# Performance work log

Measured on AMD Instinct MI355X. Metric: run time of the kernel, lower is better.

## Reference

```python
import jax, jax.numpy as jnp
import numpy as np

B, EVI, L, H, K, NL = 16, 5, 128, 768, 21, 3
SIGMA = 0.1

def _kernel_mus(n):
    mu = [1.0]
    bin_size = 2.0 / (n - 1)
    mu.append(1 - bin_size / 2)
    for i in range(1, n - 1):
        mu.append(mu[i] - bin_size)
    return mu

MU = np.asarray(_kernel_mus(K), dtype=np.float32)                      # [K]
SIG = np.asarray([0.001] + [SIGMA] * (K - 1), dtype=np.float32)        # [K]


def setup_inputs() -> dict:
    key = jax.random.key(0)
    ks = jax.random.split(key, 8)
    std = 0.02
    inputs_hiddens = jax.random.normal(ks[0], (B, EVI, L, H), jnp.float32)
    inputs = jax.random.normal(ks[1], (B, EVI, H), jnp.float32)
    # mask_text: valid tokens with CLS (position 0) zeroed, as in torch forward
    mask_text = jnp.ones((B, EVI, L), jnp.float32).at[:, :, 0].set(0.0)
    seg = (jnp.arange(L) >= L // 2).astype(jnp.float32)  # first half = claim, second = evidence
    mask_claim = (1.0 - seg) * mask_text
    mask_evidence = seg * mask_text
    return {
        "inputs_hiddens": inputs_hiddens,
        "inputs": inputs,
        "mask_text": mask_text,
        "mask_claim": mask_claim,
        "mask_evidence": mask_evidence,
        "W_att": jax.random.normal(ks[2], (K, 1), jnp.float32) * std,
        "b_att": jnp.zeros((1,), jnp.float32),
        "W_sel": jax.random.normal(ks[3], (K, 1), jnp.float32) * std,
        "b_sel": jnp.zeros((1,), jnp.float32),
        "gat_W1": jax.random.normal(ks[4], (2 * H, 128), jnp.float32) * std,
        "gat_b1": jnp.zeros((128,), jnp.float32),
        "gat_W2": jax.random.normal(ks[5], (128, 1), jnp.float32) * std,
        "gat_b2": jnp.zeros((1,), jnp.float32),
        "inf_W": jax.random.normal(ks[6], (2 * H, NL), jnp.float32) * std,
        "inf_b": jnp.zeros((NL,), jnp.float32),
    }


def _l2norm(x):
    # F.normalize(p=2, dim=-1) with eps=1e-12
    return x / jnp.maximum(jnp.linalg.norm(x, axis=-1, keepdims=True), 1e-12)


def _kernel_pool(sim, attn_d):
    # sim: [N, Lq, Ld]; attn_d: [N, Ld]  ->  [N, Lq, K]
    # exp(-(sim - mu)^2 / (2 sigma^2)) masked by doc attention, summed over doc tokens
    pv = jnp.exp(-((sim[..., None] - MU) ** 2) / (2.0 * SIG ** 2)) * attn_d[:, None, :, None]
    return pv.sum(axis=2)


def _intersect_att(qn, dn, attn_q, attn_d, W_att, b_att):
    # token-level attention scores over q tokens: [N, Lq]
    sim = jnp.einsum('nqh,ndh->nqd', qn, dn)
    lp = jnp.log(jnp.maximum(_kernel_pool(sim, attn_d), 1e-10))  # [N, Lq, K]
    lp = (lp @ W_att + b_att)[..., 0]                            # [N, Lq]
    lp = jnp.where(attn_q == 0.0, -1e4, lp)
    return jax.nn.softmax(lp, axis=1)


def _intersect_sel(qn, dn, attn_q, attn_d, W_sel, b_sel):
    # per-pair evidence selection logit: [N, 1]
    sim = jnp.einsum('nqh,ndh->nqd', qn, dn)
    lp = jnp.log(jnp.maximum(_kernel_pool(sim, attn_d), 1e-10)) * attn_q[..., None] * 0.01
    lp = lp.sum(axis=1) / (attn_q.sum(axis=1, keepdims=True) + 1e-10)  # [N, K]
    return lp @ W_sel + b_sel


def _gat(x, W1, b1, W2, b2):
    # proj_gat: Linear(2H,128) -> ReLU -> Linear(128,1)
    return jnp.maximum(x @ W1 + b1, 0.0) @ W2 + b2


def reference(inputs_hiddens, inputs, mask_text, mask_claim, mask_evidence,
              W_att, b_att, W_sel, b_sel, gat_W1, gat_b1, gat_W2, gat_b2,
              inf_W, inf_b):
    hid = inputs_hiddens                          # [B, EVI, L, H]
    hn = _l2norm(hid)
    hn_flat = hn.reshape(-1, L, H)

    # evidence selection prior over EVI pieces
    sel = _intersect_sel(hn_flat, hn_flat,
                         mask_claim.reshape(-1, L), mask_evidence.reshape(-1, L),
                         W_sel, b_sel)
    select_prob = jax.nn.softmax(sel.reshape(B, EVI, 1), axis=1)

    att_de = []
    for i in range(EVI):  # fixed small structural loop
        own_n = hn[:, i]                           # [B, L, H]
        own_mask = mask_text[:, i]                 # [B, L]
        dn = jnp.broadcast_to(own_n[:, None], (B, EVI, L, H)).reshape(-1, L, H)
        dm = jnp.broadcast_to(own_mask[:, None], (B, EVI, L)).reshape(-1, L)
        att = _intersect_att(hn_flat, dn, mask_evidence.reshape(-1, L), dm, W_att, b_att)
        att = att.reshape(B, EVI, L, 1)
        denoise = (att * hid).sum(axis=2)          # [B, EVI, H]
        own_inp = jnp.broadcast_to(inputs[:, i:i + 1], (B, EVI, H))
        w_de = jax.nn.softmax(_gat(jnp.concatenate([own_inp, denoise], -1),
                                   gat_W1, gat_b1, gat_W2, gat_b2), axis=1)  # [B, EVI, 1]
        att_de.append((denoise * w_de).sum(axis=1))  # [B, H]

    att_de = jnp.stack(att_de, axis=1)             # [B, EVI, H]
    feats = jnp.concatenate([inputs, att_de], axis=-1)  # [B, EVI, 2H]
    class_prob = jax.nn.softmax(feats @ inf_W + inf_b, axis=2)
    prob = jnp.log((select_prob * class_prob).sum(axis=1))  # [B, NL]
    return prob
```

## Files before the change

kernel.cpp:

```cpp
#include <hip/hip_runtime.h>
#include <math.h>

#define NB 16
#define NE 5
#define LL 128
#define HH 768
#define NK 21
#define NCLS 3
#define NN (NB*NE)

typedef float f32x4 __attribute__((ext_vector_type(4)));
typedef float f32x8 __attribute__((ext_vector_type(8)));
typedef short s16x8 __attribute__((ext_vector_type(8)));

__device__ __forceinline__ short bf16rne(float f) {
    union { float f; unsigned u; } c; c.f = f;
    unsigned u = c.u;
    unsigned r = (u + 0x7FFFu + ((u >> 16) & 1u)) >> 16;
    return (short)r;
}
__device__ __forceinline__ float sum8(f32x8 x) {
    return ((x[0] + x[1]) + (x[2] + x[3])) + ((x[4] + x[5]) + (x[6] + x[7]));
}
__device__ __forceinline__ f32x8 exp2v(f32x8 x) {
// ... 22 lines not shown
        const int bb = blockIdx.x - 640;
        const int tI = bb >> 1, jI = bb & 1;
        #pragma unroll
        for (int i = 0; i < 16; ++i) {
            const int r = (tid >> 6) + i * 4, c = tid & 63;
            sT[r][c] = W1[(size_t)(tI * 64 + r) * 128 + jI * 64 + c];
        }
        __syncthreads();
        #pragma unroll
        for (int i = 0; i < 16; ++i) {
            const int r = (tid >> 6) + i * 4, c = tid & 63;
            w1t[(size_t)(jI * 64 + r) * 1536 + tI * 64 + c] = sT[c][r];
        }
        return;
    }
    const int n = blockIdx.x >> 3, slab = blockIdx.x & 7;
    const int l = tid & 63, w = tid >> 6;
    float* sInv = &sT[0][0];
    #pragma unroll
    for (int rr = 0; rr < 4; ++rr) {
        const int lr = w * 4 + rr;
        const int row = slab * 16 + lr;
        const float4* rp = reinterpret_cast<const float4*>(hid + ((size_t)n * LL + row) * HH);
        float4 a = rp[l], b = rp[l + 64], c = rp[l + 128];
        float ss = a.x*a.x + a.y*a.y + a.z*a.z + a.w*a.w
                 + b.x*b.x + b.y*b.y + b.z*b.z + b.w*b.w
                 + c.x*c.x + c.y*c.y + c.z*c.z + c.w*c.w;
        #pragma unroll
        for (int o = 32; o > 0; o >>= 1) ss += __shfl_xor(ss, o, 64);
        if (l == 0) sInv[lr] = 1.0f / fmaxf(sqrtf(ss), 1e-12f);
    }
    __syncthreads();
    const float* base = hid + (size_t)n * LL * HH;
    s16x8* dst = reinterpret_cast<s16x8*>(hswz) + (size_t)n * 12288;
    #pragma unroll
    for (int i = 0; i < 6; ++i) {
        const int uid = i * 256 + tid;
        const int s = uid >> 6, sub = uid & 63;
        const int r15 = sub >> 2, kc = sub & 3;
        const int row = slab * 16 + r15;
        const int k0 = s * 32 + kc * 8;
        const float4* p = reinterpret_cast<const float4*>(base + (size_t)row * HH + k0);
        float4 v0 = p[0], v1 = p[1];
        const float inv = sInv[r15];
        s16x8 h;
        h[0] = bf16rne(v0.x * inv); h[1] = bf16rne(v0.y * inv);
        h[2] = bf16rne(v0.z * inv); h[3] = bf16rne(v0.w * inv);
        h[4] = bf16rne(v1.x * inv); h[5] = bf16rne(v1.y * inv);
        h[6] = bf16rne(v1.z * inv); h[7] = bf16rne(v1.w * inv);
        dst[(size_t)s * 512 + slab * 64 + kc * 16 + r15] = h;
    }
}

__global__ __launch_bounds__(256, 2) void k_simpool(
    const short* __restrict__ hswz,
    const float* __restrict__ mask_text, const float* __restrict__ mask_claim,
    const float* __restrict__ mask_evidence,
    const float* __restrict__ W_att, const float* __restrict__ b_att,
    const float* __restrict__ W_sel,
    float* __restrict__ attw, float2* __restrict__ dselPart)
{
    const int bid = blockIdx.x;
    const int b = bid & 15, rest = bid >> 4;
    const int pair = rest >> 1, qh = rest & 1;
    const int e = pair / NE, ep = pair - e * NE;
    const int nq = b * NE + e, nd = b * NE + ep;
    const bool diag = (e == ep);
    const int tid = threadIdx.x, lane = tid & 63, w = tid >> 6;
    const int lx = lane & 15, lg = lane >> 4;
    const int rw = w & 1, cw = w >> 1;

    __shared__ s16x8 sB[2][1024];
    __shared__ __align__(16) float sMT[LL];
    __shared__ __align__(16) float sMEd[LL];
    __shared__ float sMEq[64], sMCq[64], sSel[64];
    __shared__ float sWA[NK], sWS[NK], sCK[NK];

    if (tid < 128) {
        sMT[tid]  = mask_text[nd * LL + tid];
        sMEd[tid] = mask_evidence[nd * LL + tid];
    } else if (tid < 192) {
        const int q = tid - 128;
        sMEq[q] = mask_evidence[nq * LL + qh * 64 + q];
        sMCq[q] = mask_claim[nq * LL + qh * 64 + q];
    } else if (tid < 192 + NK) {
        sWA[tid - 192] = W_att[tid - 192] * 0.69314718f;
    } else if (tid < 213 + NK) {
        sWS[tid - 213] = W_sel[tid - 213] * 0.69314718f;
    } else if (tid < 254) {
        const int k = tid - 233;
        const float kk = (float)(k - 1);
        sCK[k] = exp2f(fmaf(kk, 13.7056029f, fmaf(kk * kk, -0.72134752f, -32.0f)));
    } else if (tid == 254) {
        sCK[0] = 1.0f;
    }

    const s16x8* gA = reinterpret_cast<const s16x8*>(hswz) + (size_t)nq * 12288;
    const s16x8* gB = reinterpret_cast<const s16x8*>(hswz) + (size_t)nd * 12288;

    const int rt0 = (qh * 4 + rw * 2) * 64;
    const int rt1 = rt0 + 64;

    {
        s16x8 t0 = gB[tid], t1 = gB[tid + 256], t2 = gB[tid + 512], t3 = gB[tid + 768];
        sB[0][tid] = t0; sB[0][tid + 256] = t1;
        sB[0][tid + 512] = t2; sB[0][tid + 768] = t3;
    }
    s16x8 a00 = gA[rt0 + lane],       a01 = gA[512 + rt0 + lane];
    s16x8 a10 = gA[rt1 + lane],       a11 = gA[512 + rt1 + lane];

    f32x4 acc[2][4];
    #pragma unroll
    for (int mi = 0; mi < 2; ++mi)
        #pragma unroll
        for (int j = 0; j < 4; ++j) acc[mi][j] = (f32x4){0.f, 0.f, 0.f, 0.f};

    __syncthreads();

    const int cb = cw * 256;
    for (int s = 0; s < 12; ++s) {
        const int cur = s & 1;
        s16x8 nB0, nB1, nB2, nB3, n00, n01, n10, n11;
        if (s < 11) {
            const s16x8* gBs = gB + (s + 1) * 1024;
            nB0 = gBs[tid]; nB1 = gBs[tid + 256];
            nB2 = gBs[tid + 512]; nB3 = gBs[tid + 768];
            const s16x8* gAs = gA + (s + 1) * 1024;
            n00 = gAs[rt0 + lane]; n01 = gAs[512 + rt0 + lane];
            n10 = gAs[rt1 + lane]; n11 = gAs[512 + rt1 + lane];
        }
        #pragma unroll
        for (int j = 0; j < 4; ++j) {
            s16x8 b0 = sB[cur][cb + j * 64 + lane];
            acc[0][j] = __builtin_amdgcn_mfma_f32_16x16x32_bf16(a00, b0, acc[0][j], 0, 0, 0);
            acc[1][j] = __builtin_amdgcn_mfma_f32_16x16x32_bf16(a10, b0, acc[1][j], 0, 0, 0);
        }
        #pragma unroll
        for (int j = 0; j < 4; ++j) {
            s16x8 b1 = sB[cur][512 + cb + j * 64 + lane];
            acc[0][j] = __builtin_amdgcn_mfma_f32_16x16x32_bf16(a01, b1, acc[0][j], 0, 0, 0);
            acc[1][j] = __builtin_amdgcn_mfma_f32_16x16x32_bf16(a11, b1, acc[1][j], 0, 0, 0);
        }
        if (s < 11) {
            sB[1 - cur][tid] = nB0; sB[1 - cur][tid + 256] = nB1;
            sB[1 - cur][tid + 512] = nB2; sB[1 - cur][tid + 768] = nB3;
            a00 = n00; a01 = n01; a10 = n10; a11 = n11;
            __syncthreads();
        }
    }

    __syncthreads();
    float* sS = reinterpret_cast<float*>(sB);
    {
        #pragma unroll
        for (int mi = 0; mi < 2; ++mi) {
            #pragma unroll
            for (int j = 0; j < 4; ++j) {
                const int col = cw * 64 + j * 16 + lx;
                const int uu = col >> 2, ce = col & 3;
                #pragma unroll
                for (int r = 0; r < 4; ++r) {
                    const int row = rw * 32 + mi * 16 + lg * 4 + r;
                    sS[row * 128 + ((uu ^ (row & 31)) << 2) + ce] = acc[mi][j][r];
                }
            }
        }
    }
    __syncthreads();

    const int row = w * 16 + (lane & 15);
    const int sl  = lane >> 4;
    const int rx  = row & 31;
    const float4* rp = reinterpret_cast<const float4*>(sS + row * 128);

    float pk[NK], vk[NK];
    #pragma unroll
    for (int k = 0; k < NK; ++k) { pk[k] = 0.f; vk[k] = 0.f; }

    #pragma unroll
    for (int c = 0; c < 4; ++c) {
        const float4 va = rp[(sl * 8 + c * 2) ^ rx];
        const float4 vb = rp[(sl * 8 + c * 2 + 1) ^ rx];
        const f32x8 s = mk8(va, vb);
        const int j0 = sl * 32 + c * 8;
        const f32x8 m = mk8(*reinterpret_cast<const float4*>(&sMT[j0]),
                            *reinterpret_cast<const float4*>(&sMT[j0 + 4]));
        f32x8 d = s - 1.0f;
        const f32x8 g = exp2v(d * d * -721347.52f);
        pk[0] += sum8(m * g);
        const f32x8 t = exp2v(s * -14.4269504f);
        d = s - 0.95f;
        const f32x8 P = exp2v(d * d * -72.134752f + 32.0f);
        f32x8 u = m * P;
        pk[1] += sum8(u);
        #pragma unroll
        for (int k = 2; k <= 20; ++k) { u *= t; pk[k] += sum8(u); }
        if (diag) {
            const f32x8 me = mk8(*reinterpret_cast<const float4*>(&sMEd[j0]),
                                 *reinterpret_cast<const float4*>(&sMEd[j0 + 4]));
            f32x8 uv = me * P;
            vk[0] += sum8(me * g);
            vk[1] += sum8(uv);
            #pragma unroll
            for (int k = 2; k <= 20; ++k) { uv *= t; vk[k] += sum8(uv); }
        }
    }
    #pragma unroll
    for (int k = 0; k < NK; ++k) {
        pk[k] += __shfl_xor(pk[k], 16, 64);
        pk[k] += __shfl_xor(pk[k], 32, 64);
    }
    if (diag) {
        #pragma unroll
        for (int k = 0; k < NK; ++k) {
            vk[k] += __shfl_xor(vk[k], 16, 64);
            vk[k] += __shfl_xor(vk[k], 32, 64);
        }
    }
    const float bAtt = b_att[0];
    float lgt = bAtt;
    #pragma unroll
    for (int k = 0; k < NK; ++k)
        lgt = fmaf(sWA[k], log2f(fmaxf(pk[k] * sCK[k], 1e-10f)), lgt);
    if (sl == 0) {
        const size_t obase = ((size_t)ep * NN + nq) * LL + qh * 64;
        attw[obase + row] = (sMEq[row] == 0.0f) ? -10000.0f : lgt;
    }
    if (diag) {
        float rv = 0.f;
        #pragma unroll
        for (int k = 0; k < NK; ++k)
            rv = fmaf(sWS[k], log2f(fmaxf(vk[k] * sCK[k], 1e-10f)), rv);
        if (sl == 0) sSel[row] = sMCq[row] * rv;
        __syncthreads();
        if (tid < 64) {
            float su = sSel[tid], ms = sMCq[tid];
            #pragma unroll
            for (int o = 32; o > 0; o >>= 1) {
                su += __shfl_xor(su, o, 64);
                ms += __shfl_xor(ms, o, 64);
            }
            if (tid == 0) dselPart[nq * 2 + qh] = make_float2(su, ms);
        }
    }
}

__global__ __launch_bounds__(256) void k_denoise(
    const float* __restrict__ hid, const float* __restrict__ attw,
    float* __restrict__ denoi)
{
    const int blk = blockIdx.x;
    const int nq = blk / 3, ch = blk - nq * 3;
    const int tid = threadIdx.x, l = tid & 63, g = tid >> 6;
    __shared__ float sA[NE][LL];
    __shared__ f32x4 sP[4][NE][64];
    for (int ep = g; ep < NE; ep += 4) {
        const float* ap = attw + ((size_t)ep * NN + nq) * LL;
        float a0 = ap[l], a1 = ap[l + 64];
        float m = fmaxf(a0, a1);
        #pragma unroll
        for (int o = 32; o > 0; o >>= 1) m = fmaxf(m, __shfl_xor(m, o, 64));
        float e0 = __expf(a0 - m), e1 = __expf(a1 - m);
        float s = e0 + e1;
        #pragma unroll
        for (int o = 32; o > 0; o >>= 1) s += __shfl_xor(s, o, 64);
        float inv = 1.0f / s;
        sA[ep][l] = e0 * inv;
        sA[ep][l + 64] = e1 * inv;
    }
    __syncthreads();
    const int h = ch * 256 + l * 4;
    const f32x4* hp = reinterpret_cast<const f32x4*>(hid + (size_t)nq * LL * HH + h);
    f32x4 p0 = {0,0,0,0}, p1 = {0,0,0,0}, p2 = {0,0,0,0}, p3 = {0,0,0,0}, p4 = {0,0,0,0};
    #pragma unroll 8
    for (int q = 0; q < 32; ++q) {
        const int qq = g * 32 + q;
        const f32x4 x = hp[(size_t)qq * (HH / 4)];
        p0 += sA[0][qq] * x;
        p1 += sA[1][qq] * x;
        p2 += sA[2][qq] * x;
        p3 += sA[3][qq] * x;
        p4 += sA[4][qq] * x;
    }
    sP[g][0][l] = p0; sP[g][1][l] = p1; sP[g][2][l] = p2;
    sP[g][3][l] = p3; sP[g][4][l] = p4;
    __syncthreads();
    if (tid < 64) {
        #define DNST(EP) { \
            f32x4 r = sP[0][EP][l] + sP[1][EP][l] + sP[2][EP][l] + sP[3][EP][l]; \
            *reinterpret_cast<f32x4*>(denoi + ((size_t)(EP) * NN + nq) * HH + h) = r; }
        DNST(0) DNST(1) DNST(2) DNST(3) DNST(4)
        #undef DNST
    }
}

// ... 126 lines not shown
    float d0, d1, d2, d3, d4;
#define DSEL(I, D) { float2 pa = dselPart[(b * NE + (I)) * 2], pb = dselPart[(b * NE + (I)) * 2 + 1]; \
                     (D) = bs + 0.01f * (pa.x + pb.x) / ((pa.y + pb.y) + 1e-10f); }
    DSEL(0, d0) DSEL(1, d1) DSEL(2, d2) DSEL(3, d3) DSEL(4, d4)
#undef DSEL
    float m = fmaxf(fmaxf(fmaxf(d0, d1), fmaxf(d2, d3)), d4);
    float s0 = __expf(d0 - m), s1 = __expf(d1 - m), s2 = __expf(d2 - m);
    float s3 = __expf(d3 - m), s4 = __expf(d4 - m);
    float sinv = 1.0f / (s0 + s1 + s2 + s3 + s4);
    float sp0 = s0 * sinv, sp1 = s1 * sinv, sp2 = s2 * sinv, sp3 = s3 * sinv, sp4 = s4 * sinv;
    float acc0 = 0.f, acc1 = 0.f, acc2 = 0.f;
#define CMB(I, SP) { \
        float l0 = logi[(b * NE + (I)) * NCLS], l1 = logi[(b * NE + (I)) * NCLS + 1], \
              l2 = logi[(b * NE + (I)) * NCLS + 2]; \
        float mm = fmaxf(fmaxf(l0, l1), l2); \
        float e0 = __expf(l0 - mm), e1 = __expf(l1 - mm), e2 = __expf(l2 - mm); \
        float si = 1.0f / (e0 + e1 + e2); \
        acc0 += (SP) * e0 * si; acc1 += (SP) * e1 * si; acc2 += (SP) * e2 * si; }
    CMB(0, sp0) CMB(1, sp1) CMB(2, sp2) CMB(3, sp3) CMB(4, sp4)
#undef CMB
    out[b * NCLS + 0] = logf(acc0);
    out[b * NCLS + 1] = logf(acc1);
    out[b * NCLS + 2] = logf(acc2);
}

extern "C" void kernel_launch(void* const* d_in, const int* in_sizes, int n_in,
                              void* d_out, int out_size, void* d_ws, size_t ws_size,
                              hipStream_t stream) {
    (void)in_sizes; (void)n_in; (void)out_size; (void)ws_size;
    const float* hid           = (const float*)d_in[0];
    const float* inputs        = (const float*)d_in[1];
    const float* mask_text     = (const float*)d_in[2];
    const float* mask_claim    = (const float*)d_in[3];
    const float* mask_evidence = (const float*)d_in[4];
    const float* W_att  = (const float*)d_in[5];
    const float* b_att  = (const float*)d_in[6];
    const float* W_sel  = (const float*)d_in[7];
    const float* b_sel  = (const float*)d_in[8];
    const float* gat_W1 = (const float*)d_in[9];
    const float* gat_b1 = (const float*)d_in[10];
    const float* gat_W2 = (const float*)d_in[11];
    const float* gat_b2 = (const float*)d_in[12];
    const float* inf_W  = (const float*)d_in[13];
    const float* inf_b  = (const float*)d_in[14];
    (void)gat_b2;

    short* hswz  = (short*)d_ws;
    float* denoi = (float*)((char*)d_ws + 15728640);
    float* attw  = denoi + 307200;
    float2* dselPart = (float2*)(attw + 51200);
    float* w1t   = (float*)(dselPart + 160);
    float* part  = w1t + 196608;
    float* logi  = part + 25600;

    k_prep<<<688, 256, 0, stream>>>(hid, hswz, gat_W1, w1t);
    k_simpool<<<800, 256, 0, stream>>>(hswz, mask_text, mask_claim, mask_evidence,
                                       W_att, b_att, W_sel, attw, dselPart);
    k_denoise<<<NN * 3, 256, 0, stream>>>(hid, attw, denoi);
    k_gat2<<<800, 256, 0, stream>>>(inputs, denoi, w1t, gat_b1, gat_W2, part);
    k_logits<<<NN, 256, 0, stream>>>(inputs, denoi, part, inf_W, inf_b, logi);
    k_combine<<<1, 64, 0, stream>>>(dselPart, b_sel, logi, (float*)d_out);
}
```

Baseline: 81.67 us.

## Split fused similarity GEMM and kernel pooling into two separate kernels

Splits the fused k_simpool kernel in two. k_gemm computes the bf16 MFMA similarity tiles and writes them to a global scratch buffer, and k_pool reads them back to do the Gaussian kernel pooling and logits. The intent is to stop the GEMM's register and LDS pressure from capping occupancy in the exp-heavy pooling phase, and to let each kernel get its own launch bounds. The cost is an extra launch plus a round trip of about 6.5 MB of fp32 similarities through global memory or L2.

```diff
diff --git a/kernel.cpp b/kernel.cpp
--- a/kernel.cpp
+++ b/kernel.cpp
@@ -98,8 +98,105 @@
     }
 }
 
-__global__ __launch_bounds__(256, 2) void k_simpool(
-    const short* __restrict__ hswz,
+__global__ __launch_bounds__(256, 2) void k_gemm(
+    const short* __restrict__ hswz, float* __restrict__ sims)
+{
+    const int bid = blockIdx.x;
+    const int b = bid & 15, rest = bid >> 4;
+    const int pair = rest >> 1, qh = rest & 1;
+    const int e = pair / NE, ep = pair - e * NE;
+    const int nq = b * NE + e, nd = b * NE + ep;
+    const int tid = threadIdx.x, lane = tid & 63, w = tid >> 6;
+    const int lx = lane & 15, lg = lane >> 4;
+    const int rw = w & 1, cw = w >> 1;
+
+    __shared__ s16x8 sB[2][1024];
+
+    const s16x8* gA = reinterpret_cast<const s16x8*>(hswz) + (size_t)nq * 12288;
+    const s16x8* gB = reinterpret_cast<const s16x8*>(hswz) + (size_t)nd * 12288;
+
+    const int rt0 = (qh * 4 + rw * 2) * 64;
+    const int rt1 = rt0 + 64;
+
+    {
+        s16x8 t0 = gB[tid], t1 = gB[tid + 256], t2 = gB[tid + 512], t3 = gB[tid + 768];
+        sB[0][tid] = t0; sB[0][tid + 256] = t1;
+        sB[0][tid + 512] = t2; sB[0][tid + 768] = t3;
+    }
+    s16x8 a00 = gA[rt0 + lane],       a01 = gA[512 + rt0 + lane];
+    s16x8 a10 = gA[rt1 + lane],       a11 = gA[512 + rt1 + lane];
+
+    f32x4 acc[2][4];
+    #pragma unroll
+    for (int mi = 0; mi < 2; ++mi)
+        #pragma unroll
+        for (int j = 0; j < 4; ++j) acc[mi][j] = (f32x4){0.f, 0.f, 0.f, 0.f};
+
+    __syncthreads();
+
+    const int cb = cw * 256;
+    for (int s = 0; s < 12; ++s) {
+        const int cur = s & 1;
+        s16x8 nB0, nB1, nB2, nB3, n00, n01, n10, n11;
+        if (s < 11) {
+            const s16x8* gBs = gB + (s + 1) * 1024;
+            nB0 = gBs[tid]; nB1 = gBs[tid + 256];
+            nB2 = gBs[tid + 512]; nB3 = gBs[tid + 768];
+            const s16x8* gAs = gA + (s + 1) * 1024;
+            n00 = gAs[rt0 + lane]; n01 = gAs[512 + rt0 + lane];
+            n10 = gAs[rt1 + lane]; n11 = gAs[512 + rt1 + lane];
+        }
+        #pragma unroll
+        for (int j = 0; j < 4; ++j) {
+            s16x8 b0 = sB[cur][cb + j * 64 + lane];
+            acc[0][j] = __builtin_amdgcn_mfma_f32_16x16x32_bf16(a00, b0, acc[0][j], 0, 0, 0);
+            acc[1][j] = __builtin_amdgcn_mfma_f32_16x16x32_bf16(a10, b0, acc[1][j], 0, 0, 0);
+        }
+        #pragma unroll
+        for (int j = 0; j < 4; ++j) {
+            s16x8 b1 = sB[cur][512 + cb + j * 64 + lane];
+            acc[0][j] = __builtin_amdgcn_mfma_f32_16x16x32_bf16(a01, b1, acc[0][j], 0, 0, 0);
+            acc[1][j] = __builtin_amdgcn_mfma_f32_16x16x32_bf16(a11, b1, acc[1][j], 0, 0, 0);
+        }
+        if (s < 11) {
+            sB[1 - cur][tid] = nB0; sB[1 - cur][tid + 256] = nB1;
+            sB[1 - cur][tid + 512] = nB2; sB[1 - cur][tid + 768] = nB3;
+            a00 = n00; a01 = n01; a10 = n10; a11 = n11;
+            __syncthreads();
+        }
+    }
+
+    __syncthreads();
+    float* sS = reinterpret_cast<float*>(sB);
+    {
+        #pragma unroll
+        for (int mi = 0; mi < 2; ++mi) {
+            #pragma unroll
+            for (int j = 0; j < 4; ++j) {
+                const int col = cw * 64 + j * 16 + lx;
+                const int uu = col >> 2, ce = col & 3;
+                #pragma unroll
+                for (int r = 0; r < 4; ++r) {
+                    const int row = rw * 32 + mi * 16 + lg * 4 + r;
+                    sS[row * 128 + ((uu ^ (row & 31)) << 2) + ce] = acc[mi][j][r];
+                }
+            }
+        }
+    }
+    __syncthreads();
+    float4* gs = reinterpret_cast<float4*>(sims) + (size_t)bid * 2048;
+    #pragma unroll
+    for (int k = 0; k < 8; ++k) {
+        const int q = tid + k * 256;
+        const int row = q >> 5, uu = q & 31;
+        const float4 v = *reinterpret_cast<const float4*>(
+            &sS[row * 128 + ((uu ^ (row & 31)) << 2)]);
+        gs[q] = v;
+    }
+}
+
+__global__ __launch_bounds__(256) void k_pool(
+    const float* __restrict__ sims,
     const float* __restrict__ mask_text, const float* __restrict__ mask_claim,
     const float* __restrict__ mask_evidence,
     const float* __restrict__ W_att, const float* __restrict__ b_att,
@@ -113,10 +210,7 @@
     const int nq = b * NE + e, nd = b * NE + ep;
     const bool diag = (e == ep);
     const int tid = threadIdx.x, lane = tid & 63, w = tid >> 6;
-    const int lx = lane & 15, lg = lane >> 4;
-    const int rw = w & 1, cw = w >> 1;
-
-    __shared__ s16x8 sB[2][1024];
+
     __shared__ __align__(16) float sMT[LL];
     __shared__ __align__(16) float sMEd[LL];
     __shared__ float sMEq[64], sMCq[64], sSel[64];
@@ -140,84 +234,12 @@
     } else if (tid == 254) {
         sCK[0] = 1.0f;
     }
-
-    const s16x8* gA = reinterpret_cast<const s16x8*>(hswz) + (size_t)nq * 12288;
-    const s16x8* gB = reinterpret_cast<const s16x8*>(hswz) + (size_t)nd * 12288;
-
-    const int rt0 = (qh * 4 + rw * 2) * 64;
-    const int rt1 = rt0 + 64;
-
-    {
-        s16x8 t0 = gB[tid], t1 = gB[tid + 256], t2 = gB[tid + 512], t3 = gB[tid + 768];
-        sB[0][tid] = t0; sB[0][tid + 256] = t1;
-        sB[0][tid + 512] = t2; sB[0][tid + 768] = t3;
-    }
-    s16x8 a00 = gA[rt0 + lane],       a01 = gA[512 + rt0 + lane];
-    s16x8 a10 = gA[rt1 + lane],       a11 = gA[512 + rt1 + lane];
-
-    f32x4 acc[2][4];
-    #pragma unroll
-    for (int mi = 0; mi < 2; ++mi)
-        #pragma unroll
-        for (int j = 0; j < 4; ++j) acc[mi][j] = (f32x4){0.f, 0.f, 0.f, 0.f};
-
-    __syncthreads();
-
-    const int cb = cw * 256;
-    for (int s = 0; s < 12; ++s) {
-        const int cur = s & 1;
-        s16x8 nB0, nB1, nB2, nB3, n00, n01, n10, n11;
-        if (s < 11) {
-            const s16x8* gBs = gB + (s + 1) * 1024;
-            nB0 = gBs[tid]; nB1 = gBs[tid + 256];
-            nB2 = gBs[tid + 512]; nB3 = gBs[tid + 768];
-            const s16x8* gAs = gA + (s + 1) * 1024;
-            n00 = gAs[rt0 + lane]; n01 = gAs[512 + rt0 + lane];
-            n10 = gAs[rt1 + lane]; n11 = gAs[512 + rt1 + lane];
-        }
-        #pragma unroll
-        for (int j = 0; j < 4; ++j) {
-            s16x8 b0 = sB[cur][cb + j * 64 + lane];
-            acc[0][j] = __builtin_amdgcn_mfma_f32_16x16x32_bf16(a00, b0, acc[0][j], 0, 0, 0);
-            acc[1][j] = __builtin_amdgcn_mfma_f32_16x16x32_bf16(a10, b0, acc[1][j], 0, 0, 0);
-        }
-        #pragma unroll
-        for (int j = 0; j < 4; ++j) {
-            s16x8 b1 = sB[cur][512 + cb + j * 64 + lane];
-            acc[0][j] = __builtin_amdgcn_mfma_f32_16x16x32_bf16(a01, b1, acc[0][j], 0, 0, 0);
-            acc[1][j] = __builtin_amdgcn_mfma_f32_16x16x32_bf16(a11, b1, acc[1][j], 0, 0, 0);
-        }
-        if (s < 11) {
-            sB[1 - cur][tid] = nB0; sB[1 - cur][tid + 256] = nB1;
-            sB[1 - cur][tid + 512] = nB2; sB[1 - cur][tid + 768] = nB3;
-            a00 = n00; a01 = n01; a10 = n10; a11 = n11;
-            __syncthreads();
-        }
-    }
-
-    __syncthreads();
-    float* sS = reinterpret_cast<float*>(sB);
-    {
-        #pragma unroll
-        for (int mi = 0; mi < 2; ++mi) {
-            #pragma unroll
-            for (int j = 0; j < 4; ++j) {
-                const int col = cw * 64 + j * 16 + lx;
-                const int uu = col >> 2, ce = col & 3;
-                #pragma unroll
-                for (int r = 0; r < 4; ++r) {
-                    const int row = rw * 32 + mi * 16 + lg * 4 + r;
-                    sS[row * 128 + ((uu ^ (row & 31)) << 2) + ce] = acc[mi][j][r];
-                }
-            }
-        }
-    }
-    __syncthreads();
-
-    const int row = w * 16 + (lane & 15);
-    const int sl  = lane >> 4;
-    const int rx  = row & 31;
-    const float4* rp = reinterpret_cast<const float4*>(sS + row * 128);
+    __syncthreads();
+
+    const int row = w * 16 + (lane >> 2);
+    const int sl  = lane & 3;
+    const float4* rp4 = reinterpret_cast<const float4*>(sims)
+                      + (size_t)bid * 2048 + row * 32;
 
     float pk[NK], vk[NK];
     #pragma unroll
@@ -225,8 +247,8 @@
 
     #pragma unroll
     for (int c = 0; c < 4; ++c) {
-        const float4 va = rp[(sl * 8 + c * 2) ^ rx];
-        const float4 vb = rp[(sl * 8 + c * 2 + 1) ^ rx];
+        const float4 va = rp4[sl * 8 + c * 2];
+        const float4 vb = rp4[sl * 8 + c * 2 + 1];
         const f32x8 s = mk8(va, vb);
         const int j0 = sl * 32 + c * 8;
         const f32x8 m = mk8(*reinterpret_cast<const float4*>(&sMT[j0]),
@@ -253,14 +275,14 @@
     }
     #pragma unroll
     for (int k = 0; k < NK; ++k) {
-        pk[k] += __shfl_xor(pk[k], 16, 64);
-        pk[k] += __shfl_xor(pk[k], 32, 64);
+        pk[k] += __shfl_xor(pk[k], 1, 64);
+        pk[k] += __shfl_xor(pk[k], 2, 64);
     }
     if (diag) {
         #pragma unroll
         for (int k = 0; k < NK; ++k) {
-            vk[k] += __shfl_xor(vk[k], 16, 64);
-            vk[k] += __shfl_xor(vk[k], 32, 64);
+            vk[k] += __shfl_xor(vk[k], 1, 64);
+            vk[k] += __shfl_xor(vk[k], 2, 64);
         }
     }
     const float bAtt = b_att[0];
@@ -519,10 +541,12 @@
     float* w1t   = (float*)(dselPart + 160);
     float* part  = w1t + 196608;
     float* logi  = part + 25600;
+    float* sims  = logi + 256;
 
     k_prep<<<688, 256, 0, stream>>>(hid, hswz, gat_W1, w1t);
-    k_simpool<<<800, 256, 0, stream>>>(hswz, mask_text, mask_claim, mask_evidence,
-                                       W_att, b_att, W_sel, attw, dselPart);
+    k_gemm<<<800, 256, 0, stream>>>(hswz, sims);
+    k_pool<<<800, 256, 0, stream>>>(sims, mask_text, mask_claim, mask_evidence,
+                                    W_att, b_att, W_sel, attw, dselPart);
     k_denoise<<<NN * 3, 256, 0, stream>>>(hid, attw, denoi);
     k_gat2<<<800, 256, 0, stream>>>(inputs, denoi, w1t, gat_b1, gat_W2, part);
     k_logits<<<NN, 256, 0, stream>>>(inputs, denoi, part, inf_W, inf_b, logi);
```

Result: slower. 90.36 us (+10.6%).

## Process both query halves per block in simpool to reuse staged doc tiles

Applied to the files above, without the earlier changes.

Each k_simpool block now computes all 128 query rows for a (batch, query-evidence, doc-evidence) triple instead of one 64-row half. The grid halves from 800 to 400 blocks. Each block keeps twice as many MFMA accumulators and A fragments, then runs the kernel-pooling epilogue in two phases through the same shared buffer. This halves the global loads and LDS staging of the document B tiles. The cost is higher register pressure under launch_bounds(256,2), fewer blocks to spread over the CUs, and a longer serial epilogue per block.

```diff
diff --git a/kernel.cpp b/kernel.cpp
--- a/kernel.cpp
+++ b/kernel.cpp
@@ -107,8 +107,7 @@
     float* __restrict__ attw, float2* __restrict__ dselPart)
 {
     const int bid = blockIdx.x;
-    const int b = bid & 15, rest = bid >> 4;
-    const int pair = rest >> 1, qh = rest & 1;
+    const int b = bid & 15, pair = bid >> 4;
     const int e = pair / NE, ep = pair - e * NE;
     const int nq = b * NE + e, nd = b * NE + ep;
     const bool diag = (e == ep);
@@ -119,174 +118,192 @@
     __shared__ s16x8 sB[2][1024];
     __shared__ __align__(16) float sMT[LL];
     __shared__ __align__(16) float sMEd[LL];
-    __shared__ float sMEq[64], sMCq[64], sSel[64];
+    __shared__ float sMEq[LL], sMCq[LL], sSel[64];
     __shared__ float sWA[NK], sWS[NK], sCK[NK];
 
     if (tid < 128) {
         sMT[tid]  = mask_text[nd * LL + tid];
         sMEd[tid] = mask_evidence[nd * LL + tid];
-    } else if (tid < 192) {
+    } else {
         const int q = tid - 128;
-        sMEq[q] = mask_evidence[nq * LL + qh * 64 + q];
-        sMCq[q] = mask_claim[nq * LL + qh * 64 + q];
-    } else if (tid < 192 + NK) {
-        sWA[tid - 192] = W_att[tid - 192] * 0.69314718f;
-    } else if (tid < 213 + NK) {
-        sWS[tid - 213] = W_sel[tid - 213] * 0.69314718f;
-    } else if (tid < 254) {
-        const int k = tid - 233;
+        sMEq[q] = mask_evidence[nq * LL + q];
+        sMCq[q] = mask_claim[nq * LL + q];
+    }
+    if (tid < NK) {
+        sWA[tid] = W_att[tid] * 0.69314718f;
+    } else if (tid < 2 * NK) {
+        sWS[tid - NK] = W_sel[tid - NK] * 0.69314718f;
+    } else if (tid < 62) {
+        const int k = tid - 41;
         const float kk = (float)(k - 1);
         sCK[k] = exp2f(fmaf(kk, 13.7056029f, fmaf(kk * kk, -0.72134752f, -32.0f)));
-    } else if (tid == 254) {
+    } else if (tid == 62) {
         sCK[0] = 1.0f;
     }
 
     const s16x8* gA = reinterpret_cast<const s16x8*>(hswz) + (size_t)nq * 12288;
     const s16x8* gB = reinterpret_cast<const s16x8*>(hswz) + (size_t)nd * 12288;
 
-    const int rt0 = (qh * 4 + rw * 2) * 64;
-    const int rt1 = rt0 + 64;
+    const int rt00 = (rw * 2) * 64,     rt01 = rt00 + 64;
+    const int rt10 = (4 + rw * 2) * 64, rt11 = rt10 + 64;
 
     {
         s16x8 t0 = gB[tid], t1 = gB[tid + 256], t2 = gB[tid + 512], t3 = gB[tid + 768];
         sB[0][tid] = t0; sB[0][tid + 256] = t1;
         sB[0][tid + 512] = t2; sB[0][tid + 768] = t3;
     }
-    s16x8 a00 = gA[rt0 + lane],       a01 = gA[512 + rt0 + lane];
-    s16x8 a10 = gA[rt1 + lane],       a11 = gA[512 + rt1 + lane];
-
-    f32x4 acc[2][4];
-    #pragma unroll
-    for (int mi = 0; mi < 2; ++mi)
-        #pragma unroll
-        for (int j = 0; j < 4; ++j) acc[mi][j] = (f32x4){0.f, 0.f, 0.f, 0.f};
+    s16x8 a000 = gA[rt00 + lane], a001 = gA[512 + rt00 + lane];
+    s16x8 a010 = gA[rt01 + lane], a011 = gA[512 + rt01 + lane];
+    s16x8 a100 = gA[rt10 + lane], a101 = gA[512 + rt10 + lane];
+    s16x8 a110 = gA[rt11 + lane], a111 = gA[512 + rt11 + lane];
+
+    f32x4 acc[2][2][4];
+    #pragma unroll
+    for (int h = 0; h < 2; ++h)
+        #pragma unroll
+        for (int mi = 0; mi < 2; ++mi)
+            #pragma unroll
+            for (int j = 0; j < 4; ++j) acc[h][mi][j] = (f32x4){0.f, 0.f, 0.f, 0.f};
 
     __syncthreads();
 
     const int cb = cw * 256;
     for (int s = 0; s < 12; ++s) {
         const int cur = s & 1;
-        s16x8 nB0, nB1, nB2, nB3, n00, n01, n10, n11;
+        s16x8 nB0, nB1, nB2, nB3;
+        s16x8 n000, n001, n010, n011, n100, n101, n110, n111;
         if (s < 11) {
             const s16x8* gBs = gB + (s + 1) * 1024;
             nB0 = gBs[tid]; nB1 = gBs[tid + 256];
             nB2 = gBs[tid + 512]; nB3 = gBs[tid + 768];
             const s16x8* gAs = gA + (s + 1) * 1024;
-            n00 = gAs[rt0 + lane]; n01 = gAs[512 + rt0 + lane];
-            n10 = gAs[rt1 + lane]; n11 = gAs[512 + rt1 + lane];
+            n000 = gAs[rt00 + lane]; n001 = gAs[512 + rt00 + lane];
+            n010 = gAs[rt01 + lane]; n011 = gAs[512 + rt01 + lane];
+            n100 = gAs[rt10 + lane]; n101 = gAs[512 + rt10 + lane];
+            n110 = gAs[rt11 + lane]; n111 = gAs[512 + rt11 + lane];
         }
         #pragma unroll
         for (int j = 0; j < 4; ++j) {
-            s16x8 b0 = sB[cur][cb + j * 64 + lane];
-            acc[0][j] = __builtin_amdgcn_mfma_f32_16x16x32_bf16(a00, b0, acc[0][j], 0, 0, 0);
-            acc[1][j] = __builtin_amdgcn_mfma_f32_16x16x32_bf16(a10, b0, acc[1][j], 0, 0, 0);
+            s16x8 bf = sB[cur][cb + j * 64 + lane];
+            acc[0][0][j] = __builtin_amdgcn_mfma_f32_16x16x32_bf16(a000, bf, acc[0][0][j], 0, 0, 0);
+            acc[0][1][j] = __builtin_amdgcn_mfma_f32_16x16x32_bf16(a010, bf, acc[0][1][j], 0, 0, 0);
+            acc[1][0][j] = __builtin_amdgcn_mfma_f32_16x16x32_bf16(a100, bf, acc[1][0][j], 0, 0, 0);
+            acc[1][1][j] = __builtin_amdgcn_mfma_f32_16x16x32_bf16(a110, bf, acc[1][1][j], 0, 0, 0);
         }
         #pragma unroll
         for (int j = 0; j < 4; ++j) {
-            s16x8 b1 = sB[cur][512 + cb + j * 64 + lane];
-            acc[0][j] = __builtin_amdgcn_mfma_f32_16x16x32_bf16(a01, b1, acc[0][j], 0, 0, 0);
-            acc[1][j] = __builtin_amdgcn_mfma_f32_16x16x32_bf16(a11, b1, acc[1][j], 0, 0, 0);
+            s16x8 bf = sB[cur][512 + cb + j * 64 + lane];
+            acc[0][0][j] = __builtin_amdgcn_mfma_f32_16x16x32_bf16(a001, bf, acc[0][0][j], 0, 0, 0);
+            acc[0][1][j] = __builtin_amdgcn_mfma_f32_16x16x32_bf16(a011, bf, acc[0][1][j], 0, 0, 0);
+            acc[1][0][j] = __builtin_amdgcn_mfma_f32_16x16x32_bf16(a101, bf, acc[1][0][j], 0, 0, 0);
+            acc[1][1][j] = __builtin_amdgcn_mfma_f32_16x16x32_bf16(a111, bf, acc[1][1][j], 0, 0, 0);
         }
         if (s < 11) {
             sB[1 - cur][tid] = nB0; sB[1 - cur][tid + 256] = nB1;
             sB[1 - cur][tid + 512] = nB2; sB[1 - cur][tid + 768] = nB3;
-            a00 = n00; a01 = n01; a10 = n10; a11 = n11;
+            a000 = n000; a001 = n001; a010 = n010; a011 = n011;
+            a100 = n100; a101 = n101; a110 = n110; a111 = n111;
             __syncthreads();
         }
     }
 
-    __syncthreads();
     float* sS = reinterpret_cast<float*>(sB);
-    {
-        #pragma unroll
-        for (int mi = 0; mi < 2; ++mi) {
+    const float bAtt = b_att[0];
+    const size_t obase = ((size_t)ep * NN + nq) * LL;
+
+    #pragma unroll
+    for (int ph = 0; ph < 2; ++ph) {
+        __syncthreads();
+        {
             #pragma unroll
-            for (int j = 0; j < 4; ++j) {
-                const int col = cw * 64 + j * 16 + lx;
-                const int uu = col >> 2, ce = col & 3;
+            for (int mi = 0; mi < 2; ++mi) {
                 #pragma unroll
-                for (int r = 0; r < 4; ++r) {
-                    const int row = rw * 32 + mi * 16 + lg * 4 + r;
-                    sS[row * 128 + ((uu ^ (row & 31)) << 2) + ce] = acc[mi][j][r];
+                for (int j = 0; j < 4; ++j) {
+                    const int col = cw * 64 + j * 16 + lx;
+                    const int uu = col >> 2, ce = col & 3;
+                    #pragma unroll
+                    for (int r = 0; r < 4; ++r) {
+                        const int row = rw * 32 + mi * 16 + lg * 4 + r;
+                        const f32x4 av = (ph == 0) ? acc[0][mi][j] : acc[1][mi][j];
+                        sS[row * 128 + ((uu ^ (row & 31)) << 2) + ce] = av[r];
+                    }
                 }
             }
         }
-    }
-    __syncthreads();
-
-    const int row = w * 16 + (lane & 15);
-    const int sl  = lane >> 4;
-    const int rx  = row & 31;
-    const float4* rp = reinterpret_cast<const float4*>(sS + row * 128);
-
-    float pk[NK], vk[NK];
-    #pragma unroll
-    for (int k = 0; k < NK; ++k) { pk[k] = 0.f; vk[k] = 0.f; }
-
-    #pragma unroll
-    for (int c = 0; c < 4; ++c) {
-        const float4 va = rp[(sl * 8 + c * 2) ^ rx];
-        const float4 vb = rp[(sl * 8 + c * 2 + 1) ^ rx];
-        const f32x8 s = mk8(va, vb);
-        const int j0 = sl * 32 + c * 8;
-        const f32x8 m = mk8(*reinterpret_cast<const float4*>(&sMT[j0]),
-                            *reinterpret_cast<const float4*>(&sMT[j0 + 4]));
-        f32x8 d = s - 1.0f;
-        const f32x8 g = exp2v(d * d * -721347.52f);
-        pk[0] += sum8(m * g);
-        const f32x8 t = exp2v(s * -14.4269504f);
-        d = s - 0.95f;
-        const f32x8 P = exp2v(d * d * -72.134752f + 32.0f);
-        f32x8 u = m * P;
-        pk[1] += sum8(u);
-        #pragma unroll
-        for (int k = 2; k <= 20; ++k) { u *= t; pk[k] += sum8(u); }
+        __syncthreads();
+
+        const int row = w * 16 + (lane & 15);
+        const int sl  = lane >> 4;
+        const int rx  = row & 31;
+        const int grow = ph * 64 + row;
+        const float4* rp = reinterpret_cast<const float4*>(sS + row * 128);
+
+        float pk[NK], vk[NK];
+        #pragma unroll
+        for (int k = 0; k < NK; ++k) { pk[k] = 0.f; vk[k] = 0.f; }
+
+        #pragma unroll
+        for (int c = 0; c < 4; ++c) {
+            const float4 va = rp[(sl * 8 + c * 2) ^ rx];
+            const float4 vb = rp[(sl * 8 + c * 2 + 1) ^ rx];
+            const f32x8 s = mk8(va, vb);
+            const int j0 = sl * 32 + c * 8;
+            const f32x8 m = mk8(*reinterpret_cast<const float4*>(&sMT[j0]),
+                                *reinterpret_cast<const float4*>(&sMT[j0 + 4]));
+            f32x8 d = s - 1.0f;
+            const f32x8 g = exp2v(d * d * -721347.52f);
+            pk[0] += sum8(m * g);
+            const f32x8 t = exp2v(s * -14.4269504f);
+            d = s - 0.95f;
+            const f32x8 P = exp2v(d * d * -72.134752f + 32.0f);
+            f32x8 u = m * P;
+            pk[1] += sum8(u);
+            #pragma unroll
+            for (int k = 2; k <= 20; ++k) { u *= t; pk[k] += sum8(u); }
+            if (diag) {
+                const f32x8 me = mk8(*reinterpret_cast<const float4*>(&sMEd[j0]),
+                                     *reinterpret_cast<const float4*>(&sMEd[j0 + 4]));
+                f32x8 uv = me * P;
+                vk[0] += sum8(me * g);
+                vk[1] += sum8(uv);
+                #pragma unroll
+                for (int k = 2; k <= 20; ++k) { uv *= t; vk[k] += sum8(uv); }
+            }
+        }
+        #pragma unroll
+        for (int k = 0; k < NK; ++k) {
+            pk[k] += __shfl_xor(pk[k], 16, 64);
+            pk[k] += __shfl_xor(pk[k], 32, 64);
+        }
         if (diag) {
-            const f32x8 me = mk8(*reinterpret_cast<const float4*>(&sMEd[j0]),
-                                 *reinterpret_cast<const float4*>(&sMEd[j0 + 4]));
-            f32x8 uv = me * P;
-            vk[0] += sum8(me * g);
-            vk[1] += sum8(uv);
             #pragma unroll
-            for (int k = 2; k <= 20; ++k) { uv *= t; vk[k] += sum8(uv); }
-        }
-    }
-    #pragma unroll
-    for (int k = 0; k < NK; ++k) {
-        pk[k] += __shfl_xor(pk[k], 16, 64);
-        pk[k] += __shfl_xor(pk[k], 32, 64);
-    }
-    if (diag) {
-        #pragma unroll
-        for (int k = 0; k < NK; ++k) {
-            vk[k] += __shfl_xor(vk[k], 16, 64);
-            vk[k] += __shfl_xor(vk[k], 32, 64);
-        }
-    }
-    const float bAtt = b_att[0];
-    float lgt = bAtt;
-    #pragma unroll
-    for (int k = 0; k < NK; ++k)
-        lgt = fmaf(sWA[k], log2f(fmaxf(pk[k] * sCK[k], 1e-10f)), lgt);
-    if (sl == 0) {
-        const size_t obase = ((size_t)ep * NN + nq) * LL + qh * 64;
-        attw[obase + row] = (sMEq[row] == 0.0f) ? -10000.0f : lgt;
-    }
-    if (diag) {
-        float rv = 0.f;
+            for (int k = 0; k < NK; ++k) {
+                vk[k] += __shfl_xor(vk[k], 16, 64);
+                vk[k] += __shfl_xor(vk[k], 32, 64);
+            }
+        }
+        float lgt = bAtt;
         #pragma unroll
         for (int k = 0; k < NK; ++k)
-            rv = fmaf(sWS[k], log2f(fmaxf(vk[k] * sCK[k], 1e-10f)), rv);
-        if (sl == 0) sSel[row] = sMCq[row] * rv;
-        __syncthreads();
-        if (tid < 64) {
-            float su = sSel[tid], ms = sMCq[tid];
+            lgt = fmaf(sWA[k], log2f(fmaxf(pk[k] * sCK[k], 1e-10f)), lgt);
+        if (sl == 0)
+            attw[obase + grow] = (sMEq[grow] == 0.0f) ? -10000.0f : lgt;
+        if (diag) {
+            float rv = 0.f;
             #pragma unroll
-            for (int o = 32; o > 0; o >>= 1) {
-                su += __shfl_xor(su, o, 64);
-                ms += __shfl_xor(ms, o, 64);
+            for (int k = 0; k < NK; ++k)
+                rv = fmaf(sWS[k], log2f(fmaxf(vk[k] * sCK[k], 1e-10f)), rv);
+            if (sl == 0) sSel[row] = sMCq[grow] * rv;
+            __syncthreads();
+            if (tid < 64) {
+                float su = sSel[tid], ms = sMCq[ph * 64 + tid];
+                #pragma unroll
+                for (int o = 32; o > 0; o >>= 1) {
+                    su += __shfl_xor(su, o, 64);
+                    ms += __shfl_xor(ms, o, 64);
+                }
+                if (tid == 0) dselPart[nq * 2 + ph] = make_float2(su, ms);
             }
-            if (tid == 0) dselPart[nq * 2 + qh] = make_float2(su, ms);
         }
     }
 }
@@ -521,7 +538,7 @@
     float* logi  = part + 25600;
 
     k_prep<<<688, 256, 0, stream>>>(hid, hswz, gat_W1, w1t);
-    k_simpool<<<800, 256, 0, stream>>>(hswz, mask_text, mask_claim, mask_evidence,
+    k_simpool<<<400, 256, 0, stream>>>(hswz, mask_text, mask_claim, mask_evidence,
                                        W_att, b_att, W_sel, attw, dselPart);
     k_denoise<<<NN * 3, 256, 0, stream>>>(hid, attw, denoi);
     k_gat2<<<800, 256, 0, stream>>>(inputs, denoi, w1t, gat_b1, gat_W2, part);
```

Measured after the change: 83.13 us. About the same (+1.8%).

## Merge query halves into one 512-thread simpool block sharing doc tiles

Applied to the files above, without the earlier changes.

k_simpool now handles all 128 query rows of a (query, doc) pair in one 512-thread block instead of splitting them across two 256-thread blocks. The doc B tile is loaded into shared memory once per pair instead of twice, which halves global and LDS staging traffic for B. The kernel-pooling epilogue runs in two phases through the same shared scratch, with eight lanes per row. The cost is fewer blocks (400), extra barriers between phases, and possible register pressure at the larger launch bound.

```diff
diff --git a/kernel.cpp b/kernel.cpp
--- a/kernel.cpp
+++ b/kernel.cpp
@@ -98,7 +98,7 @@
     }
 }
 
-__global__ __launch_bounds__(256, 2) void k_simpool(
+__global__ __launch_bounds__(512, 2) void k_simpool(
     const short* __restrict__ hswz,
     const float* __restrict__ mask_text, const float* __restrict__ mask_claim,
     const float* __restrict__ mask_evidence,
@@ -107,53 +107,51 @@
     float* __restrict__ attw, float2* __restrict__ dselPart)
 {
     const int bid = blockIdx.x;
-    const int b = bid & 15, rest = bid >> 4;
-    const int pair = rest >> 1, qh = rest & 1;
+    const int b = bid & 15, pair = bid >> 4;
     const int e = pair / NE, ep = pair - e * NE;
     const int nq = b * NE + e, nd = b * NE + ep;
     const bool diag = (e == ep);
     const int tid = threadIdx.x, lane = tid & 63, w = tid >> 6;
     const int lx = lane & 15, lg = lane >> 4;
-    const int rw = w & 1, cw = w >> 1;
+    const int rw = w & 3, cw = w >> 2;
 
     __shared__ s16x8 sB[2][1024];
     __shared__ __align__(16) float sMT[LL];
     __shared__ __align__(16) float sMEd[LL];
-    __shared__ float sMEq[64], sMCq[64], sSel[64];
+    __shared__ float sMEq[LL], sMCq[LL], sSel[64];
     __shared__ float sWA[NK], sWS[NK], sCK[NK];
 
     if (tid < 128) {
         sMT[tid]  = mask_text[nd * LL + tid];
         sMEd[tid] = mask_evidence[nd * LL + tid];
-    } else if (tid < 192) {
+    } else if (tid < 256) {
         const int q = tid - 128;
-        sMEq[q] = mask_evidence[nq * LL + qh * 64 + q];
-        sMCq[q] = mask_claim[nq * LL + qh * 64 + q];
-    } else if (tid < 192 + NK) {
-        sWA[tid - 192] = W_att[tid - 192] * 0.69314718f;
-    } else if (tid < 213 + NK) {
-        sWS[tid - 213] = W_sel[tid - 213] * 0.69314718f;
-    } else if (tid < 254) {
-        const int k = tid - 233;
+        sMEq[q] = mask_evidence[nq * LL + q];
+        sMCq[q] = mask_claim[nq * LL + q];
+    } else if (tid < 256 + NK) {
+        sWA[tid - 256] = W_att[tid - 256] * 0.69314718f;
+    } else if (tid >= 288 && tid < 288 + NK) {
+        sWS[tid - 288] = W_sel[tid - 288] * 0.69314718f;
+    } else if (tid >= 320 && tid < 340) {
+        const int k = tid - 319;
         const float kk = (float)(k - 1);
         sCK[k] = exp2f(fmaf(kk, 13.7056029f, fmaf(kk * kk, -0.72134752f, -32.0f)));
-    } else if (tid == 254) {
+    } else if (tid == 340) {
         sCK[0] = 1.0f;
     }
 
     const s16x8* gA = reinterpret_cast<const s16x8*>(hswz) + (size_t)nq * 12288;
     const s16x8* gB = reinterpret_cast<const s16x8*>(hswz) + (size_t)nd * 12288;
 
-    const int rt0 = (qh * 4 + rw * 2) * 64;
+    const int rt0 = (rw * 2) * 64;
     const int rt1 = rt0 + 64;
 
     {
-        s16x8 t0 = gB[tid], t1 = gB[tid + 256], t2 = gB[tid + 512], t3 = gB[tid + 768];
-        sB[0][tid] = t0; sB[0][tid + 256] = t1;
-        sB[0][tid + 512] = t2; sB[0][tid + 768] = t3;
-    }
-    s16x8 a00 = gA[rt0 + lane],       a01 = gA[512 + rt0 + lane];
-    s16x8 a10 = gA[rt1 + lane],       a11 = gA[512 + rt1 + lane];
+        s16x8 t0 = gB[tid], t1 = gB[tid + 512];
+        sB[0][tid] = t0; sB[0][tid + 512] = t1;
+    }
+    s16x8 a00 = gA[rt0 + lane], a01 = gA[512 + rt0 + lane];
+    s16x8 a10 = gA[rt1 + lane], a11 = gA[512 + rt1 + lane];
 
     f32x4 acc[2][4];
     #pragma unroll
@@ -166,127 +164,131 @@
     const int cb = cw * 256;
     for (int s = 0; s < 12; ++s) {
         const int cur = s & 1;
-        s16x8 nB0, nB1, nB2, nB3, n00, n01, n10, n11;
+        s16x8 nB0, nB1, n00, n01, n10, n11;
         if (s < 11) {
             const s16x8* gBs = gB + (s + 1) * 1024;
-            nB0 = gBs[tid]; nB1 = gBs[tid + 256];
-            nB2 = gBs[tid + 512]; nB3 = gBs[tid + 768];
+            nB0 = gBs[tid]; nB1 = gBs[tid + 512];
             const s16x8* gAs = gA + (s + 1) * 1024;
             n00 = gAs[rt0 + lane]; n01 = gAs[512 + rt0 + lane];
             n10 = gAs[rt1 + lane]; n11 = gAs[512 + rt1 + lane];
         }
         #pragma unroll
         for (int j = 0; j < 4; ++j) {
-            s16x8 b0 = sB[cur][cb + j * 64 + lane];
-            acc[0][j] = __builtin_amdgcn_mfma_f32_16x16x32_bf16(a00, b0, acc[0][j], 0, 0, 0);
-            acc[1][j] = __builtin_amdgcn_mfma_f32_16x16x32_bf16(a10, b0, acc[1][j], 0, 0, 0);
+            s16x8 bf = sB[cur][cb + j * 64 + lane];
+            acc[0][j] = __builtin_amdgcn_mfma_f32_16x16x32_bf16(a00, bf, acc[0][j], 0, 0, 0);
+            acc[1][j] = __builtin_amdgcn_mfma_f32_16x16x32_bf16(a10, bf, acc[1][j], 0, 0, 0);
         }
         #pragma unroll
         for (int j = 0; j < 4; ++j) {
-            s16x8 b1 = sB[cur][512 + cb + j * 64 + lane];
-            acc[0][j] = __builtin_amdgcn_mfma_f32_16x16x32_bf16(a01, b1, acc[0][j], 0, 0, 0);
-            acc[1][j] = __builtin_amdgcn_mfma_f32_16x16x32_bf16(a11, b1, acc[1][j], 0, 0, 0);
+            s16x8 bf = sB[cur][512 + cb + j * 64 + lane];
+            acc[0][j] = __builtin_amdgcn_mfma_f32_16x16x32_bf16(a01, bf, acc[0][j], 0, 0, 0);
+            acc[1][j] = __builtin_amdgcn_mfma_f32_16x16x32_bf16(a11, bf, acc[1][j], 0, 0, 0);
         }
         if (s < 11) {
-            sB[1 - cur][tid] = nB0; sB[1 - cur][tid + 256] = nB1;
-            sB[1 - cur][tid + 512] = nB2; sB[1 - cur][tid + 768] = nB3;
+            sB[1 - cur][tid] = nB0; sB[1 - cur][tid + 512] = nB1;
             a00 = n00; a01 = n01; a10 = n10; a11 = n11;
             __syncthreads();
         }
     }
 
-    __syncthreads();
     float* sS = reinterpret_cast<float*>(sB);
-    {
-        #pragma unroll
-        for (int mi = 0; mi < 2; ++mi) {
+    const float bAtt = b_att[0];
+    const size_t obase = ((size_t)ep * NN + nq) * LL;
+    const int rloc = w * 8 + (lane >> 3);
+    const int sl   = lane & 7;
+    const int rx   = rloc & 31;
+
+    #pragma unroll
+    for (int ph = 0; ph < 2; ++ph) {
+        __syncthreads();
+        if ((rw >> 1) == ph) {
             #pragma unroll
-            for (int j = 0; j < 4; ++j) {
-                const int col = cw * 64 + j * 16 + lx;
-                const int uu = col >> 2, ce = col & 3;
+            for (int mi = 0; mi < 2; ++mi) {
                 #pragma unroll
-                for (int r = 0; r < 4; ++r) {
-                    const int row = rw * 32 + mi * 16 + lg * 4 + r;
-                    sS[row * 128 + ((uu ^ (row & 31)) << 2) + ce] = acc[mi][j][r];
+                for (int j = 0; j < 4; ++j) {
+                    const int col = cw * 64 + j * 16 + lx;
+                    const int uu = col >> 2, ce = col & 3;
+                    #pragma unroll
+                    for (int r = 0; r < 4; ++r) {
+                        const int rl = (rw & 1) * 32 + mi * 16 + lg * 4 + r;
+                        sS[rl * 128 + ((uu ^ (rl & 31)) << 2) + ce] = acc[mi][j][r];
+                    }
                 }
             }
         }
-    }
-    __syncthreads();
-
-    const int row = w * 16 + (lane & 15);
-    const int sl  = lane >> 4;
-    const int rx  = row & 31;
-    const float4* rp = reinterpret_cast<const float4*>(sS + row * 128);
-
-    float pk[NK], vk[NK];
-    #pragma unroll
-    for (int k = 0; k < NK; ++k) { pk[k] = 0.f; vk[k] = 0.f; }
-
-    #pragma unroll
-    for (int c = 0; c < 4; ++c) {
-        const float4 va = rp[(sl * 8 + c * 2) ^ rx];
-        const float4 vb = rp[(sl * 8 + c * 2 + 1) ^ rx];
-        const f32x8 s = mk8(va, vb);
-        const int j0 = sl * 32 + c * 8;
-        const f32x8 m = mk8(*reinterpret_cast<const float4*>(&sMT[j0]),
-                            *reinterpret_cast<const float4*>(&sMT[j0 + 4]));
-        f32x8 d = s - 1.0f;
-        const f32x8 g = exp2v(d * d * -721347.52f);
-        pk[0] += sum8(m * g);
-        const f32x8 t = exp2v(s * -14.4269504f);
-        d = s - 0.95f;
-        const f32x8 P = exp2v(d * d * -72.134752f + 32.0f);
-        f32x8 u = m * P;
-        pk[1] += sum8(u);
-        #pragma unroll
-        for (int k = 2; k <= 20; ++k) { u *= t; pk[k] += sum8(u); }
+        __syncthreads();
+
+        const int grow = ph * 64 + rloc;
+        const float4* rp4 = reinterpret_cast<const float4*>(sS + rloc * 128);
+
+        float pk[NK], vk[NK];
+        #pragma unroll
+        for (int k = 0; k < NK; ++k) { pk[k] = 0.f; vk[k] = 0.f; }
+
+        #pragma unroll
+        for (int c = 0; c < 2; ++c) {
+            const float4 va = rp4[(sl * 4 + c * 2) ^ rx];
+            const float4 vb = rp4[(sl * 4 + c * 2 + 1) ^ rx];
+            const f32x8 s = mk8(va, vb);
+            const int j0 = sl * 16 + c * 8;
+            const f32x8 m = mk8(*reinterpret_cast<const float4*>(&sMT[j0]),
+                                *reinterpret_cast<const float4*>(&sMT[j0 + 4]));
+            f32x8 d = s - 1.0f;
+            const f32x8 g = exp2v(d * d * -721347.52f);
+            pk[0] += sum8(m * g);
+            const f32x8 t = exp2v(s * -14.4269504f);
+            d = s - 0.95f;
+            const f32x8 P = exp2v(d * d * -72.134752f + 32.0f);
+            f32x8 u = m * P;
+            pk[1] += sum8(u);
+            #pragma unroll
+            for (int k = 2; k <= 20; ++k) { u *= t; pk[k] += sum8(u); }
+            if (diag) {
+                const f32x8 me = mk8(*reinterpret_cast<const float4*>(&sMEd[j0]),
+                                     *reinterpret_cast<const float4*>(&sMEd[j0 + 4]));
+                f32x8 uv = me * P;
+                vk[0] += sum8(me * g);
+                vk[1] += sum8(uv);
+                #pragma unroll
+                for (int k = 2; k <= 20; ++k) { uv *= t; vk[k] += sum8(uv); }
+            }
+        }
+        #pragma unroll
+        for (int k = 0; k < NK; ++k) {
+            pk[k] += __shfl_xor(pk[k], 1, 64);
+            pk[k] += __shfl_xor(pk[k], 2, 64);
+            pk[k] += __shfl_xor(pk[k], 4, 64);
+        }
         if (diag) {
-            const f32x8 me = mk8(*reinterpret_cast<const float4*>(&sMEd[j0]),
-                                 *reinterpret_cast<const float4*>(&sMEd[j0 + 4]));
-            f32x8 uv = me * P;
-            vk[0] += sum8(me * g);
-            vk[1] += sum8(uv);
             #pragma unroll
-            for (int k = 2; k <= 20; ++k) { uv *= t; vk[k] += sum8(uv); }
-        }
-    }
-    #pragma unroll
-    for (int k = 0; k < NK; ++k) {
-        pk[k] += __shfl_xor(pk[k], 16, 64);
-        pk[k] += __shfl_xor(pk[k], 32, 64);
-    }
-    if (diag) {
-        #pragma unroll
-        for (int k = 0; k < NK; ++k) {
-            vk[k] += __shfl_xor(vk[k], 16, 64);
-            vk[k] += __shfl_xor(vk[k], 32, 64);
-        }
-    }
-    const float bAtt = b_att[0];
-    float lgt = bAtt;
-    #pragma unroll
-    for (int k = 0; k < NK; ++k)
-        lgt = fmaf(sWA[k], log2f(fmaxf(pk[k] * sCK[k], 1e-10f)), lgt);
-    if (sl == 0) {
-        const size_t obase = ((size_t)ep * NN + nq) * LL + qh * 64;
-        attw[obase + row] = (sMEq[row] == 0.0f) ? -10000.0f : lgt;
-    }
-    if (diag) {
-        float rv = 0.f;
+            for (int k = 0; k < NK; ++k) {
+                vk[k] += __shfl_xor(vk[k], 1, 64);
+                vk[k] += __shfl_xor(vk[k], 2, 64);
+                vk[k] += __shfl_xor(vk[k], 4, 64);
+            }
+        }
+        float lgt = bAtt;
         #pragma unroll
         for (int k = 0; k < NK; ++k)
-            rv = fmaf(sWS[k], log2f(fmaxf(vk[k] * sCK[k], 1e-10f)), rv);
-        if (sl == 0) sSel[row] = sMCq[row] * rv;
-        __syncthreads();
-        if (tid < 64) {
-            float su = sSel[tid], ms = sMCq[tid];
+            lgt = fmaf(sWA[k], log2f(fmaxf(pk[k] * sCK[k], 1e-10f)), lgt);
+        if (sl == 0)
+            attw[obase + grow] = (sMEq[grow] == 0.0f) ? -10000.0f : lgt;
+        if (diag) {
+            float rv = 0.f;
             #pragma unroll
-            for (int o = 32; o > 0; o >>= 1) {
-                su += __shfl_xor(su, o, 64);
-                ms += __shfl_xor(ms, o, 64);
+            for (int k = 0; k < NK; ++k)
+                rv = fmaf(sWS[k], log2f(fmaxf(vk[k] * sCK[k], 1e-10f)), rv);
+            if (sl == 0) sSel[rloc] = sMCq[grow] * rv;
+            __syncthreads();
+            if (tid < 64) {
+                float su = sSel[tid], ms = sMCq[ph * 64 + tid];
+                #pragma unroll
+                for (int o = 32; o > 0; o >>= 1) {
+                    su += __shfl_xor(su, o, 64);
+                    ms += __shfl_xor(ms, o, 64);
+                }
+                if (tid == 0) dselPart[nq * 2 + ph] = make_float2(su, ms);
             }
-            if (tid == 0) dselPart[nq * 2 + qh] = make_float2(su, ms);
         }
     }
 }
@@ -521,7 +523,7 @@
     float* logi  = part + 25600;
 
     k_prep<<<688, 256, 0, stream>>>(hid, hswz, gat_W1, w1t);
-    k_simpool<<<800, 256, 0, stream>>>(hswz, mask_text, mask_claim, mask_evidence,
+    k_simpool<<<400, 512, 0, stream>>>(hswz, mask_text, mask_claim, mask_evidence,
                                        W_att, b_att, W_sel, attw, dselPart);
     k_denoise<<<NN * 3, 256, 0, stream>>>(hid, attw, denoi);
     k_gat2<<<800, 256, 0, stream>>>(inputs, denoi, w1t, gat_b1, gat_W2, part);
```

Result: slower. 93.68 us (+14.7%).
